# Kernel optimization log

Hardware: AMD Instinct MI355X
Metric: run time of the kernel (lower is better)

Reference implementation:

```python
import jax, jax.numpy as jnp
import numpy as np

DIM = 32
HID = 128          # edge-MLP hidden width
N = 8192           # total nodes
E = 131072         # total edges
B = 64             # number of graphs
NUM_MP = 3
S2S_STEPS = 3


def setup_inputs() -> dict:
    key = jax.random.key(0)
    ks = jax.random.split(key, 24)
    g = lambda k, shape, s=0.05: jax.random.normal(k, shape, dtype=jnp.float32) * s

    inp = {
        "x": jax.random.normal(ks[0], (N, 1), dtype=jnp.float32),
        "edge_attr": jax.random.uniform(ks[1], (E, 2), dtype=jnp.float32),
        # params
        "lin0_w": g(ks[2], (1, DIM)), "lin0_b": g(ks[3], (DIM,)),
        "enn_w1": g(ks[4], (2, HID)), "enn_b1": g(ks[5], (HID,)),
        "enn_w2": g(ks[6], (HID, DIM * DIM)), "enn_b2": g(ks[7], (DIM * DIM,)),
        "root_w": g(ks[8], (DIM, DIM)), "conv_b": g(ks[9], (DIM,)),
        # GRU (gates ordered r,z,n as in torch)
        "gru_wih": g(ks[10], (DIM, 3 * DIM)), "gru_whh": g(ks[11], (DIM, 3 * DIM)),
        "gru_bih": g(ks[12], (3 * DIM,)), "gru_bhh": g(ks[13], (3 * DIM,)),
        # Set2Set LSTM: input 2*DIM, hidden DIM (gates ordered i,f,g,o as in torch)
        "s2s_wih": g(ks[14], (2 * DIM, 4 * DIM)), "s2s_whh": g(ks[15], (DIM, 4 * DIM)),
        "s2s_bih": g(ks[16], (4 * DIM,)), "s2s_bhh": g(ks[17], (4 * DIM,)),
        "lin1_w": g(ks[18], (2 * DIM, DIM)), "lin1_b": g(ks[19], (DIM,)),
        "lin2_w": g(ks[20], (DIM, 1)), "lin2_b": g(ks[21], (1,)),
        # int args
        "edge_index": jax.random.randint(ks[22], (2, E), 0, N, dtype=jnp.int32),
        "batch": jnp.sort(jax.random.randint(ks[23], (N,), 0, B, dtype=jnp.int32)),
    }
    return inp


def _forward(x, edge_attr, lin0_w, lin0_b, enn_w1, enn_b1, enn_w2, enn_b2,
             root_w, conv_b, gru_wih, gru_whh, gru_bih, gru_bhh,
             s2s_wih, s2s_whh, s2s_bih, s2s_bhh, lin1_w, lin1_b, lin2_w, lin2_b,
             edge_index, batch):
    src, dst = edge_index[0], edge_index[1]

    out = jax.nn.relu(x @ lin0_w + lin0_b)          # [N, DIM]
    h = out                                          # GRU hidden state

    # edge-conditioned weights (constant across MP layers -> hoisted)
    ew = jax.nn.relu(edge_attr @ enn_w1 + enn_b1) @ enn_w2 + enn_b2
    W = ew.reshape(E, DIM, DIM)                      # [E, in, out]

    deg = jnp.maximum(jax.ops.segment_sum(jnp.ones((E,), jnp.float32), dst,
                                          num_segments=N), 1.0)[:, None]

    for _ in range(NUM_MP):
        # NNConv: gather -> per-edge small matmul -> scatter-mean, + root + bias
        msg = jnp.einsum('ed,edo->eo', out[src], W)  # [E, DIM]
        agg = jax.ops.segment_sum(msg, dst, num_segments=N) / deg
        m = jax.nn.relu(agg + out @ root_w + conv_b)
        # GRU cell (single step)
        gi = m @ gru_wih + gru_bih
        gh = h @ gru_whh + gru_bhh
        ir, iz, in_ = jnp.split(gi, 3, axis=-1)
        hr, hz, hn = jnp.split(gh, 3, axis=-1)
        r = jax.nn.sigmoid(ir + hr)
        z = jax.nn.sigmoid(iz + hz)
        n = jnp.tanh(in_ + r * hn)
        h = (1.0 - z) * n + z * h
        out = h

    # Set2Set pooling
    qh = jnp.zeros((B, DIM), jnp.float32)
    qc = jnp.zeros((B, DIM), jnp.float32)
    q_star = jnp.zeros((B, 2 * DIM), jnp.float32)
    for _ in range(S2S_STEPS):
        gates = q_star @ s2s_wih + s2s_bih + qh @ s2s_whh + s2s_bhh
        i_, f_, g_, o_ = jnp.split(gates, 4, axis=-1)
        qc = jax.nn.sigmoid(f_) * qc + jax.nn.sigmoid(i_) * jnp.tanh(g_)
        qh = jax.nn.sigmoid(o_) * jnp.tanh(qc)       # [B, DIM]
        e = jnp.sum(out * qh[batch], axis=-1)        # [N] attention logits
        emax = jax.ops.segment_max(e, batch, num_segments=B)
        a = jnp.exp(e - emax[batch])
        a = a / jax.ops.segment_sum(a, batch, num_segments=B)[batch]
        r_read = jax.ops.segment_sum(a[:, None] * out, batch, num_segments=B)
        q_star = jnp.concatenate([qh, r_read], axis=-1)  # [B, 2*DIM]

    y = jax.nn.relu(q_star @ lin1_w + lin1_b) @ lin2_w + lin2_b
    return y.reshape(-1)                              # [B]


def reference(x, edge_attr, lin0_w, lin0_b, enn_w1, enn_b1, enn_w2, enn_b2,
              root_w, conv_b, gru_wih, gru_whh, gru_bih, gru_bhh,
              s2s_wih, s2s_whh, s2s_bih, s2s_bhh, lin1_w, lin1_b, lin2_w, lin2_b,
              edge_index, batch):
    return _forward(x, edge_attr, lin0_w, lin0_b, enn_w1, enn_b1, enn_w2, enn_b2,
                    root_w, conv_b, gru_wih, gru_whh, gru_bih, gru_bhh,
                    s2s_wih, s2s_whh, s2s_bih, s2s_bhh, lin1_w, lin1_b, lin2_w,
                    lin2_b, edge_index, batch)
```

## Files before the change

### kernel.cpp

```cpp
#include <hip/hip_runtime.h>

#define N_NODES 8192
#define N_EDGES 131072
#define NGRAPH  64
#define DIM     32
#define HID     128
#define KFULL   128
#define KHALF   64
#define G_NODES 4
#define SROW    36

__device__ __forceinline__ float sigmoidf_(float x) { return 1.0f / (1.0f + expf(-x)); }

__global__ void prep1_kernel(const float* __restrict__ x, const float* __restrict__ w,
                             const float* __restrict__ b, float* __restrict__ out,
                             const int* __restrict__ dst, int* __restrict__ counts) {
  const int bb = blockIdx.x;
  if (bb < 1024) {
    int idx = bb * 256 + threadIdx.x;
    int n = idx >> 5, d = idx & 31;
    out[idx] = fmaxf(fmaf(x[n], w[d], b[d]), 0.0f);
  } else {
    int e = (bb - 1024) * 256 + threadIdx.x;
    atomicAdd(&counts[dst[e]], 1);
  }
}

__global__ void scan_kernel(const int* __restrict__ counts,
                            int* __restrict__ offsets,
                            float* __restrict__ deg_inv) {
  __shared__ int sm[1024];
  int t = threadIdx.x;
  int base = t * 8;
  int loc[8];
  int s = 0;
#pragma unroll
  for (int i = 0; i < 8; ++i) { loc[i] = s; s += counts[base + i]; }
  sm[t] = s;
  __syncthreads();
  for (int off = 1; off < 1024; off <<= 1) {
    int v = (t >= off) ? sm[t - off] : 0;
    __syncthreads();
    sm[t] += v;
    __syncthreads();
  }
  int excl = (t > 0) ? sm[t - 1] : 0;
#pragma unroll
  for (int i = 0; i < 8; ++i) {
    offsets[base + i] = excl + loc[i];
    int c = counts[base + i];
    deg_inv[base + i] = 1.0f / (float)(c > 0 ? c : 1);
  }
  if (t == 1023) offsets[N_NODES] = sm[1023];
}

__global__ void prep2_kernel(const int* __restrict__ ei, const float* __restrict__ ea,
                             const int* __restrict__ offsets, int* __restrict__ cursor,
                             int* __restrict__ csr_src, float2* __restrict__ csr_ea,
                             const int* __restrict__ batch, int* __restrict__ gstart) {
  const int bb = blockIdx.x;
  if (bb < 512) {
    int e = bb * 256 + threadIdx.x;
    int d = ei[N_EDGES + e];
    int pos = atomicAdd(&cursor[d], 1);
    int slot = offsets[d] + pos;
    csr_src[slot] = ei[e];
    csr_ea[slot] = make_float2(ea[2 * e], ea[2 * e + 1]);
  } else {
    int n = (bb - 512) * 256 + threadIdx.x;
    int b = batch[n];
    if (n == 0) {
      for (int g = 0; g <= b; ++g) gstart[g] = 0;
    } else {
      int bp = batch[n - 1];
      for (int g = bp + 1; g <= b; ++g) gstart[g] = n;
    }
    if (n == N_NODES - 1) {
      for (int g = b + 1; g <= NGRAPH; ++g) gstart[g] = N_NODES;
    }
  }
}

__global__ __launch_bounds__(256, 3) void mp_layer_kernel(
    const float* __restrict__ out_cur, const int* __restrict__ offsets,
    const int* __restrict__ csr_src, const float2* __restrict__ csr_ea,
    const float* __restrict__ w1, const float* __restrict__ b1,
    const float* __restrict__ w2, const float* __restrict__ b2,
    const float* __restrict__ deg_inv, const float* __restrict__ root_w,
    const float* __restrict__ conv_b, const float* __restrict__ gwih,
    const float* __restrict__ gwhh, const float* __restrict__ gbih,
    const float* __restrict__ gbhh, float* __restrict__ out_nxt) {
  constexpr int C = 32;
  __shared__ float smem[G_NODES * KHALF * SROW];
  float* S = smem;
  float* hidb = smem;
  float* osrcb = smem + C * KFULL;
  float* w1s  = smem + 5120;
  float* red = smem;
  float* ob  = smem + 4352;
  float* hb  = smem + 4480;
  float* mb  = smem + 4608;
  float* b2s = smem + 4736;
  __shared__ int offs[G_NODES + 1];

  const int t = threadIdx.x;
  const int node0 = blockIdx.x * G_NODES;

  if (t <= G_NODES) offs[t] = offsets[node0 + t];
  if (t < HID) {
    w1s[t] = w1[t];
    w1s[HID + t] = w1[HID + t];
    w1s[2 * HID + t] = b1[t];
  }

  const int kg = t >> 3, dg = t & 7;
  const int k0 = kg * 4, d0 = dg * 4;
  const int ec = t >> 3, sub = t & 7;

  float acc[G_NODES][4][4];
#pragma unroll
  for (int g = 0; g < G_NODES; ++g)
#pragma unroll
    for (int i = 0; i < 4; ++i)
#pragma unroll
      for (int j = 0; j < 4; ++j) acc[g][i][j] = 0.0f;
  float oacc[G_NODES] = {};
  __syncthreads();

#pragma unroll
  for (int g = 0; g < G_NODES; ++g) {
    const int base = offs[g], end = offs[g + 1];
    for (int c0 = base; c0 < end; c0 += C) {
      const int cnt = min(C, end - c0);
      __syncthreads();
      if (ec < cnt) {
        const int slot = c0 + ec;
        const float2 eav = csr_ea[slot];
        const int sidx = csr_src[slot];
#pragma unroll
        for (int j = 0; j < 4; ++j) {
          const float4 wx = *(const float4*)(w1s + sub * 16 + j * 4);
          const float4 wy = *(const float4*)(w1s + HID + sub * 16 + j * 4);
          const float4 wb = *(const float4*)(w1s + 2 * HID + sub * 16 + j * 4);
          float4 hv4;
          hv4.x = fmaxf(fmaf(eav.y, wy.x, fmaf(eav.x, wx.x, wb.x)), 0.0f);
          hv4.y = fmaxf(fmaf(eav.y, wy.y, fmaf(eav.x, wx.y, wb.y)), 0.0f);
          hv4.z = fmaxf(fmaf(eav.y, wy.z, fmaf(eav.x, wx.z, wb.z)), 0.0f);
          hv4.w = fmaxf(fmaf(eav.y, wy.w, fmaf(eav.x, wx.w, wb.w)), 0.0f);
          *(float4*)(hidb + ec * KFULL + sub * 16 + j * 4) = hv4;
        }
        *(float4*)(osrcb + ec * DIM + sub * 4) =
            *(const float4*)(out_cur + sidx * DIM + sub * 4);
      }
      __syncthreads();
      for (int e = 0; e < cnt; ++e) {
        const float4 hvv = *(const float4*)(hidb + e * KFULL + k0);
        const float4 ov = *(const float4*)(osrcb + e * DIM + d0);
        acc[g][0][0] = fmaf(hvv.x, ov.x, acc[g][0][0]);
        acc[g][0][1] = fmaf(hvv.x, ov.y, acc[g][0][1]);
        acc[g][0][2] = fmaf(hvv.x, ov.z, acc[g][0][2]);
        acc[g][0][3] = fmaf(hvv.x, ov.w, acc[g][0][3]);
        acc[g][1][0] = fmaf(hvv.y, ov.x, acc[g][1][0]);
        acc[g][1][1] = fmaf(hvv.y, ov.y, acc[g][1][1]);
        acc[g][1][2] = fmaf(hvv.y, ov.z, acc[g][1][2]);
        acc[g][1][3] = fmaf(hvv.y, ov.w, acc[g][1][3]);
        acc[g][2][0] = fmaf(hvv.z, ov.x, acc[g][2][0]);
        acc[g][2][1] = fmaf(hvv.z, ov.y, acc[g][2][1]);
        acc[g][2][2] = fmaf(hvv.z, ov.z, acc[g][2][2]);
        acc[g][2][3] = fmaf(hvv.z, ov.w, acc[g][2][3]);
        acc[g][3][0] = fmaf(hvv.w, ov.x, acc[g][3][0]);
        acc[g][3][1] = fmaf(hvv.w, ov.y, acc[g][3][1]);
        acc[g][3][2] = fmaf(hvv.w, ov.z, acc[g][3][2]);
        acc[g][3][3] = fmaf(hvv.w, ov.w, acc[g][3][3]);
        if (t < DIM) oacc[g] += osrcb[e * DIM + t];
      }
    }
  }
  __syncthreads();

  const int ks = t >> 4;
  const int dvh = (t >> 3) & 1;
  const int og = t & 7;
  float a4[G_NODES][4];
#pragma unroll
  for (int g = 0; g < G_NODES; ++g)
#pragma unroll
    for (int r = 0; r < 4; ++r) a4[g][r] = 0.0f;

#pragma unroll
  for (int p = 0; p < 2; ++p) {
    if ((kg >> 4) == p) {
      const int kgl4 = (kg & 15) * 4;
      const int shift = (kg & 3) * 8;
      const int dd = (d0 + shift) & 31;
#pragma unroll
      for (int g = 0; g < G_NODES; ++g) {
        float* Sg = S + g * KHALF * SROW;
#pragma unroll
        for (int i = 0; i < 4; ++i)
          *(float4*)(Sg + (kgl4 + i) * SROW + dd) =
              make_float4(acc[g][i][0], acc[g][i][1], acc[g][i][2], acc[g][i][3]);
      }
    }
    __syncthreads();
#pragma unroll
    for (int i = 0; i < 4; ++i) {
      const int kl = ks * 4 + i;
      const int shift = (ks & 3) * 8;
      const float* w2k = w2 + (size_t)(p * KHALF + kl) * (DIM * DIM);
#pragma unroll
      for (int q = 0; q < 4; ++q) {
        const int dbase = dvh * 16 + q * 4;
        const int dq = (dbase + shift) & 31;
        const int soff = kl * SROW + dq;
        const float4 sv0 = *(const float4*)(S + 0 * KHALF * SROW + soff);
        const float4 sv1 = *(const float4*)(S + 1 * KHALF * SROW + soff);
        const float4 sv2 = *(const float4*)(S + 2 * KHALF * SROW + soff);
        const float4 sv3 = *(const float4*)(S + 3 * KHALF * SROW + soff);
        const float* s0 = (const float*)&sv0;
        const float* s1 = (const float*)&sv1;
        const float* s2 = (const float*)&sv2;
        const float* s3 = (const float*)&sv3;
#pragma unroll
        for (int r = 0; r < 4; ++r) {
          const float4 wv = *(const float4*)(w2k + (dbase + r) * DIM + og * 4);
          a4[0][0] = fmaf(s0[r], wv.x, a4[0][0]);
          a4[0][1] = fmaf(s0[r], wv.y, a4[0][1]);
          a4[0][2] = fmaf(s0[r], wv.z, a4[0][2]);
          a4[0][3] = fmaf(s0[r], wv.w, a4[0][3]);
          a4[1][0] = fmaf(s1[r], wv.x, a4[1][0]);
          a4[1][1] = fmaf(s1[r], wv.y, a4[1][1]);
          a4[1][2] = fmaf(s1[r], wv.z, a4[1][2]);
          a4[1][3] = fmaf(s1[r], wv.w, a4[1][3]);
          a4[2][0] = fmaf(s2[r], wv.x, a4[2][0]);
          a4[2][1] = fmaf(s2[r], wv.y, a4[2][1]);
          a4[2][2] = fmaf(s2[r], wv.z, a4[2][2]);
          a4[2][3] = fmaf(s2[r], wv.w, a4[2][3]);
          a4[3][0] = fmaf(s3[r], wv.x, a4[3][0]);
          a4[3][1] = fmaf(s3[r], wv.y, a4[3][1]);
          a4[3][2] = fmaf(s3[r], wv.z, a4[3][2]);
          a4[3][3] = fmaf(s3[r], wv.w, a4[3][3]);
        }
      }
    }
    __syncthreads();
  }

#pragma unroll
  for (int g = 0; g < G_NODES; ++g)
#pragma unroll
    for (int r = 0; r < 4; ++r) red[(g * 4 + r) * 257 + t] = a4[g][r];
  if (t < DIM) {
#pragma unroll
    for (int g = 0; g < G_NODES; ++g) ob[g * DIM + t] = oacc[g];
  }
  if (t < G_NODES * DIM) hb[t] = out_cur[node0 * DIM + t];
#pragma unroll
  for (int i = 0; i < 4; ++i) b2s[i * 256 + t] = b2[i * 256 + t];
  __syncthreads();

  if (t < G_NODES * DIM) {
    const int g = t >> 5, o = t & 31;
    const int og2 = o >> 2, r2 = o & 3;
    const float* rp = red + (g * 4 + r2) * 257 + og2;
    float agg = 0.0f;
#pragma unroll
    for (int j = 0; j < 32; ++j) agg += rp[j * 8];
#pragma unroll
    for (int d = 0; d < DIM; ++d) agg = fmaf(ob[g * DIM + d], b2s[d * DIM + o], agg);
    agg *= deg_inv[node0 + g];
    float rt = conv_b[o];
#pragma unroll
    for (int d = 0; d < DIM; ++d) rt = fmaf(hb[g * DIM + d], root_w[d * DIM + o], rt);
    mb[t] = fmaxf(agg + rt, 0.0f);
  }
  __syncthreads();
  if (t < G_NODES * DIM) {
    const int g = t >> 5, o = t & 31;
    float gi[3], gh[3];
#pragma unroll
    for (int jj = 0; jj < 3; ++jj) {
      float si = gbih[jj * DIM + o], sh = gbhh[jj * DIM + o];
#pragma unroll
      for (int d = 0; d < DIM; ++d) {
        si = fmaf(mb[g * DIM + d], gwih[d * 3 * DIM + jj * DIM + o], si);
        sh = fmaf(hb[g * DIM + d], gwhh[d * 3 * DIM + jj * DIM + o], sh);
      }
      gi[jj] = si;
      gh[jj] = sh;
    }
    const float r = sigmoidf_(gi[0] + gh[0]);
    const float z = sigmoidf_(gi[1] + gh[1]);
    const float nn = tanhf(fmaf(r, gh[2], gi[2]));
    out_nxt[node0 * DIM + t] = (1.0f - z) * nn + z * hb[t];
  }
}

__global__ __launch_bounds__(256) void s2s_kernel(
    const float* __restrict__ outf, const int* __restrict__ gstart,
    const float* __restrict__ wih, const float* __restrict__ whh,
    const float* __restrict__ bih, const float* __restrict__ bhh,
    const float* __restrict__ l1w, const float* __restrict__ l1b,
    const float* __restrict__ l2w, const float* __restrict__ l2b,
    float* __restrict__ y) {
  __shared__ float qh[DIM], qc[DIM], qstar[2 * DIM], gates[4 * DIM];
  __shared__ float wsum[4], wmax[4], wr[4][DIM];
  const int b = blockIdx.x, t = threadIdx.x;
  const int gs = gstart[b], ge = gstart[b + 1];
  const int w = t >> 6, lane = t & 63;
  if (t < DIM) { qh[t] = 0.0f; qc[t] = 0.0f; }
  if (t < 2 * DIM) qstar[t] = 0.0f;
  __syncthreads();
  for (int step = 0; step < 3; ++step) {
    if (t < 4 * DIM) {
      float gv = bih[t] + bhh[t];
      for (int i = 0; i < 2 * DIM; ++i) gv = fmaf(qstar[i], wih[i * 4 * DIM + t], gv);
      for (int i = 0; i < DIM; ++i) gv = fmaf(qh[i], whh[i * 4 * DIM + t], gv);
      gates[t] = gv;
    }
    __syncthreads();
    if (t < DIM) {
      const float ig = sigmoidf_(gates[t]);
      const float fg = sigmoidf_(gates[DIM + t]);
      const float gg = tanhf(gates[2 * DIM + t]);
      const float og = sigmoidf_(gates[3 * DIM + t]);
      const float c = fmaf(fg, qc[t], ig * gg);
      qc[t] = c;
      qh[t] = og * tanhf(c);
    }
    __syncthreads();
    float lmax = -INFINITY;
    for (int n = gs + t; n < ge; n += 256) {
      const float* orow = outf + n * DIM;
      float e = 0.0f;
#pragma unroll
      for (int d = 0; d < DIM; ++d) e = fmaf(orow[d], qh[d], e);
      lmax = fmaxf(lmax, e);
    }
#pragma unroll
    for (int off = 32; off > 0; off >>= 1) lmax = fmaxf(lmax, __shfl_xor(lmax, off));
    if (lane == 0) wmax[w] = lmax;
    __syncthreads();
    const float gmax = fmaxf(fmaxf(wmax[0], wmax[1]), fmaxf(wmax[2], wmax[3]));
    float rl[DIM];
#pragma unroll
    for (int d = 0; d < DIM; ++d) rl[d] = 0.0f;
    float lsum = 0.0f;
    for (int n = gs + t; n < ge; n += 256) {
      const float* orow = outf + n * DIM;
      float e = 0.0f;
#pragma unroll
      for (int d = 0; d < DIM; ++d) e = fmaf(orow[d], qh[d], e);
      const float a = expf(e - gmax);
      lsum += a;
#pragma unroll
      for (int d = 0; d < DIM; ++d) rl[d] = fmaf(a, orow[d], rl[d]);
    }
#pragma unroll
    for (int off = 32; off > 0; off >>= 1) {
      lsum += __shfl_xor(lsum, off);
#pragma unroll
      for (int d = 0; d < DIM; ++d) rl[d] += __shfl_xor(rl[d], off);
    }
    __syncthreads();
    if (lane == 0) {
      wsum[w] = lsum;
#pragma unroll
      for (int d = 0; d < DIM; ++d) wr[w][d] = rl[d];
    }
    __syncthreads();
    if (t < DIM) {
      const float stot = wsum[0] + wsum[1] + wsum[2] + wsum[3];
      const float rv = wr[0][t] + wr[1][t] + wr[2][t] + wr[3][t];
      qstar[t] = qh[t];
      qstar[DIM + t] = (stot > 0.0f) ? rv / stot : 0.0f;
    }
    __syncthreads();
  }
  if (t < DIM) {
    float u = l1b[t];
    for (int i = 0; i < 2 * DIM; ++i) u = fmaf(qstar[i], l1w[i * DIM + t], u);
    u = fmaxf(u, 0.0f);
    float v = u * l2w[t];
#pragma unroll
    for (int off = 16; off > 0; off >>= 1) v += __shfl_xor(v, off);
    if (t == 0) y[b] = v + l2b[0];
  }
}

extern "C" void kernel_launch(void* const* d_in, const int* in_sizes, int n_in,
                              void* d_out, int out_size, void* d_ws, size_t ws_size,
                              hipStream_t stream) {
  const float* x        = (const float*)d_in[0];
  const float* ea       = (const float*)d_in[1];
  const float* lin0_w   = (const float*)d_in[2];
  const float* lin0_b   = (const float*)d_in[3];
  const float* enn_w1   = (const float*)d_in[4];
  const float* enn_b1   = (const float*)d_in[5];
  const float* enn_w2   = (const float*)d_in[6];
  const float* enn_b2   = (const float*)d_in[7];
  const float* root_w   = (const float*)d_in[8];
  const float* conv_b   = (const float*)d_in[9];
  const float* gru_wih  = (const float*)d_in[10];
  const float* gru_whh  = (const float*)d_in[11];
  const float* gru_bih  = (const float*)d_in[12];
  const float* gru_bhh  = (const float*)d_in[13];
  const float* s2s_wih  = (const float*)d_in[14];
  const float* s2s_whh  = (const float*)d_in[15];
  const float* s2s_bih  = (const float*)d_in[16];
  const float* s2s_bhh  = (const float*)d_in[17];
  const float* lin1_w   = (const float*)d_in[18];
  const float* lin1_b   = (const float*)d_in[19];
  const float* lin2_w   = (const float*)d_in[20];
  const float* lin2_b   = (const float*)d_in[21];
  const int*   ei       = (const int*)d_in[22];
  const int*   batch    = (const int*)d_in[23];
  float* y = (float*)d_out;

  char* p = (char*)d_ws;
  auto alloc = [&](size_t bytes) -> void* {
    void* r = (void*)p;
    p += (bytes + 255) & ~(size_t)255;
    return r;
  };
  float*  out_a   = (float*)alloc(N_NODES * DIM * 4);
  float*  out_b   = (float*)alloc(N_NODES * DIM * 4);
  int*    counts  = (int*)alloc(N_NODES * 4);
  int*    cursor  = (int*)alloc(N_NODES * 4);
  int*    offsets = (int*)alloc((N_NODES + 1) * 4);
  int*    csr_src = (int*)alloc(N_EDGES * 4);
  float2* csr_ea  = (float2*)alloc(N_EDGES * 8);
  float*  deg_inv = (float*)alloc(N_NODES * 4);
  int*    gstart  = (int*)alloc((NGRAPH + 1) * 4);
  (void)ws_size; (void)n_in; (void)in_sizes; (void)out_size;

  hipMemsetAsync(counts, 0, 2 * N_NODES * 4, stream);

  prep1_kernel<<<1024 + 512, 256, 0, stream>>>(x, lin0_w, lin0_b, out_a,
                                               ei + N_EDGES, counts);
  scan_kernel<<<1, 1024, 0, stream>>>(counts, offsets, deg_inv);
  prep2_kernel<<<512 + 32, 256, 0, stream>>>(ei, ea, offsets, cursor, csr_src,
                                             csr_ea, batch, gstart);

  const int ngroups = N_NODES / G_NODES;
  const float* cur = out_a;
  float* nxt = out_b;
  for (int layer = 0; layer < 3; ++layer) {
    mp_layer_kernel<<<ngroups, 256, 0, stream>>>(
        cur, offsets, csr_src, csr_ea, enn_w1, enn_b1, enn_w2, enn_b2,
        deg_inv, root_w, conv_b, gru_wih, gru_whh, gru_bih, gru_bhh, nxt);
    const float* tmp = cur; cur = nxt; nxt = (float*)tmp;
  }

  s2s_kernel<<<NGRAPH, 256, 0, stream>>>(cur, gstart, s2s_wih, s2s_whh, s2s_bih,
                                         s2s_bhh, lin1_w, lin1_b, lin2_w, lin2_b, y);
}
```

Measured before the change: 409.0 us.

## Double-buffer edge staging in mp_layer_kernel to overlap gather with accumulation

```diff
diff --git a/kernel.cpp b/kernel.cpp
--- a/kernel.cpp
+++ b/kernel.cpp
@@ -9,6 +9,7 @@
 #define KHALF   64
 #define G_NODES 4
 #define SROW    36
+#define BUFSZ   5120
 
 __device__ __forceinline__ float sigmoidf_(float x) { return 1.0f / (1.0f + expf(-x)); }
 
@@ -91,11 +92,9 @@
     const float* __restrict__ gwhh, const float* __restrict__ gbih,
     const float* __restrict__ gbhh, float* __restrict__ out_nxt) {
   constexpr int C = 32;
-  __shared__ float smem[G_NODES * KHALF * SROW];
+  __shared__ float smem[10624];
   float* S = smem;
-  float* hidb = smem;
-  float* osrcb = smem + C * KFULL;
-  float* w1s  = smem + 5120;
+  float* w1s = smem + 2 * BUFSZ;
   float* red = smem;
   float* ob  = smem + 4352;
   float* hb  = smem + 4480;
@@ -127,53 +126,88 @@
   float oacc[G_NODES] = {};
   __syncthreads();
 
+  int ng = 0;
+  while (ng < G_NODES && offs[ng] == offs[ng + 1]) ++ng;
+  int ns = (ng < G_NODES) ? offs[ng] : 0;
+  bool nvalid = (ng < G_NODES);
+
+  auto stage = [&](int start, int cnt, int p) {
+    if (ec < cnt) {
+      float* hidb = smem + p * BUFSZ;
+      float* osrcb = smem + p * BUFSZ + 4096;
+      const int slot = start + ec;
+      const float2 eav = csr_ea[slot];
+      const int sidx = csr_src[slot];
+#pragma unroll
+      for (int j = 0; j < 4; ++j) {
+        const float4 wx = *(const float4*)(w1s + sub * 16 + j * 4);
+        const float4 wy = *(const float4*)(w1s + HID + sub * 16 + j * 4);
+        const float4 wb = *(const float4*)(w1s + 2 * HID + sub * 16 + j * 4);
+        float4 hv4;
+        hv4.x = fmaxf(fmaf(eav.y, wy.x, fmaf(eav.x, wx.x, wb.x)), 0.0f);
+        hv4.y = fmaxf(fmaf(eav.y, wy.y, fmaf(eav.x, wx.y, wb.y)), 0.0f);
+        hv4.z = fmaxf(fmaf(eav.y, wy.z, fmaf(eav.x, wx.z, wb.z)), 0.0f);
+        hv4.w = fmaxf(fmaf(eav.y, wy.w, fmaf(eav.x, wx.w, wb.w)), 0.0f);
+        *(float4*)(hidb + ec * KFULL + sub * 16 + j * 4) = hv4;
+      }
+      *(float4*)(osrcb + ec * DIM + sub * 4) =
+          *(const float4*)(out_cur + sidx * DIM + sub * 4);
+    }
+  };
+  auto advance = [&]() {
+    ns += C;
+    if (ns >= offs[ng + 1]) {
+      do { ++ng; } while (ng < G_NODES && offs[ng] == offs[ng + 1]);
+      ns = (ng < G_NODES) ? offs[ng] : 0;
+      nvalid = (ng < G_NODES);
+    }
+  };
+
+  if (nvalid) {
+    const int cnt0 = min(C, offs[ng + 1] - ns);
+    stage(ns, cnt0, 0);
+    advance();
+  }
+  __syncthreads();
+  int cur = 0;
+
 #pragma unroll
   for (int g = 0; g < G_NODES; ++g) {
     const int base = offs[g], end = offs[g + 1];
     for (int c0 = base; c0 < end; c0 += C) {
       const int cnt = min(C, end - c0);
+      if (nvalid) {
+        const int ncnt = min(C, offs[ng + 1] - ns);
+        stage(ns, ncnt, cur ^ 1);
+        advance();
+      }
+      {
+        const float* hidb = smem + cur * BUFSZ;
+        const float* osrcb = smem + cur * BUFSZ + 4096;
+        for (int e = 0; e < cnt; ++e) {
+          const float4 hvv = *(const float4*)(hidb + e * KFULL + k0);
+          const float4 ov = *(const float4*)(osrcb + e * DIM + d0);
+          acc[g][0][0] = fmaf(hvv.x, ov.x, acc[g][0][0]);
+          acc[g][0][1] = fmaf(hvv.x, ov.y, acc[g][0][1]);
+          acc[g][0][2] = fmaf(hvv.x, ov.z, acc[g][0][2]);
+          acc[g][0][3] = fmaf(hvv.x, ov.w, acc[g][0][3]);
+          acc[g][1][0] = fmaf(hvv.y, ov.x, acc[g][1][0]);
+          acc[g][1][1] = fmaf(hvv.y, ov.y, acc[g][1][1]);
+          acc[g][1][2] = fmaf(hvv.y, ov.z, acc[g][1][2]);
+          acc[g][1][3] = fmaf(hvv.y, ov.w, acc[g][1][3]);
+          acc[g][2][0] = fmaf(hvv.z, ov.x, acc[g][2][0]);
+          acc[g][2][1] = fmaf(hvv.z, ov.y, acc[g][2][1]);
+          acc[g][2][2] = fmaf(hvv.z, ov.z, acc[g][2][2]);
+          acc[g][2][3] = fmaf(hvv.z, ov.w, acc[g][2][3]);
+          acc[g][3][0] = fmaf(hvv.w, ov.x, acc[g][3][0]);
+          acc[g][3][1] = fmaf(hvv.w, ov.y, acc[g][3][1]);
+          acc[g][3][2] = fmaf(hvv.w, ov.z, acc[g][3][2]);
+          acc[g][3][3] = fmaf(hvv.w, ov.w, acc[g][3][3]);
+          if (t < DIM) oacc[g] += osrcb[e * DIM + t];
+        }
+      }
       __syncthreads();
-      if (ec < cnt) {
-        const int slot = c0 + ec;
-        const float2 eav = csr_ea[slot];
-        const int sidx = csr_src[slot];
-#pragma unroll
-        for (int j = 0; j < 4; ++j) {
-          const float4 wx = *(const float4*)(w1s + sub * 16 + j * 4);
-          const float4 wy = *(const float4*)(w1s + HID + sub * 16 + j * 4);
-          const float4 wb = *(const float4*)(w1s + 2 * HID + sub * 16 + j * 4);
-          float4 hv4;
-          hv4.x = fmaxf(fmaf(eav.y, wy.x, fmaf(eav.x, wx.x, wb.x)), 0.0f);
-          hv4.y = fmaxf(fmaf(eav.y, wy.y, fmaf(eav.x, wx.y, wb.y)), 0.0f);
-          hv4.z = fmaxf(fmaf(eav.y, wy.z, fmaf(eav.x, wx.z, wb.z)), 0.0f);
-          hv4.w = fmaxf(fmaf(eav.y, wy.w, fmaf(eav.x, wx.w, wb.w)), 0.0f);
-          *(float4*)(hidb + ec * KFULL + sub * 16 + j * 4) = hv4;
-        }
-        *(float4*)(osrcb + ec * DIM + sub * 4) =
-            *(const float4*)(out_cur + sidx * DIM + sub * 4);
-      }
-      __syncthreads();
-      for (int e = 0; e < cnt; ++e) {
-        const float4 hvv = *(const float4*)(hidb + e * KFULL + k0);
-        const float4 ov = *(const float4*)(osrcb + e * DIM + d0);
-        acc[g][0][0] = fmaf(hvv.x, ov.x, acc[g][0][0]);
-        acc[g][0][1] = fmaf(hvv.x, ov.y, acc[g][0][1]);
-        acc[g][0][2] = fmaf(hvv.x, ov.z, acc[g][0][2]);
-        acc[g][0][3] = fmaf(hvv.x, ov.w, acc[g][0][3]);
-        acc[g][1][0] = fmaf(hvv.y, ov.x, acc[g][1][0]);
-        acc[g][1][1] = fmaf(hvv.y, ov.y, acc[g][1][1]);
-        acc[g][1][2] = fmaf(hvv.y, ov.z, acc[g][1][2]);
-        acc[g][1][3] = fmaf(hvv.y, ov.w, acc[g][1][3]);
-        acc[g][2][0] = fmaf(hvv.z, ov.x, acc[g][2][0]);
-        acc[g][2][1] = fmaf(hvv.z, ov.y, acc[g][2][1]);
-        acc[g][2][2] = fmaf(hvv.z, ov.z, acc[g][2][2]);
-        acc[g][2][3] = fmaf(hvv.z, ov.w, acc[g][2][3]);
-        acc[g][3][0] = fmaf(hvv.w, ov.x, acc[g][3][0]);
-        acc[g][3][1] = fmaf(hvv.w, ov.y, acc[g][3][1]);
-        acc[g][3][2] = fmaf(hvv.w, ov.z, acc[g][3][2]);
-        acc[g][3][3] = fmaf(hvv.w, ov.w, acc[g][3][3]);
-        if (t < DIM) oacc[g] += osrcb[e * DIM + t];
-      }
+      cur ^= 1;
     }
   }
   __syncthreads();
```

New measurement: 417.2 us. No clear change (+2.0%).
